# Performance work log

Hardware: AMD Instinct MI355X
Metric: run time of the kernel (lower is better)

Reference implementation:

```python
import jax, jax.numpy as jnp
import numpy as np
from jax.experimental.ode import odeint

B, N, D, META, H, OUT = 512, 64, 4, 4, 512, 1
RTOL, ATOL = 1e-3, 1e-5


def setup_inputs() -> dict:
    key = jax.random.key(0)
    ks = jax.random.split(key, 20)
    # x channel 0 = strictly increasing event times per sample (TIME), rest randn
    dt = jax.random.uniform(ks[0], (B, N), dtype=jnp.float32) * 0.1 + 0.01
    times = jnp.cumsum(dt, axis=1)
    feats = jax.random.normal(ks[1], (B, N, D - 1), dtype=jnp.float32)
    x = jnp.concatenate([times[..., None], feats], axis=-1)
    meta = jax.random.normal(ks[2], (B, META), dtype=jnp.float32)
    eps = jax.random.normal(ks[3], (B, H), dtype=jnp.float32)

    DIN = D + META
    s_in = 1.0 / np.sqrt(DIN)
    s_h = 1.0 / np.sqrt(H)
    p = {
        # GRU (torch layout: gates [r, z, n] stacked)
        'gru_Wih': jax.random.normal(ks[4], (3 * H, DIN), jnp.float32) * s_in,
        'gru_Whh': jax.random.normal(ks[5], (3 * H, H), jnp.float32) * s_h,
        'gru_bih': jax.random.normal(ks[6], (3 * H,), jnp.float32) * s_h,
        'gru_bhh': jax.random.normal(ks[7], (3 * H,), jnp.float32) * s_h,
        # encoder head: Linear(H,H) -> ReLU -> Linear(H,2H)
        'enc_W1': jax.random.normal(ks[8], (H, H), jnp.float32) * s_h,
        'enc_b1': jax.random.normal(ks[9], (H,), jnp.float32) * s_h,
        'enc_W2': jax.random.normal(ks[10], (2 * H, H), jnp.float32) * s_h,
        'enc_b2': jax.random.normal(ks[11], (2 * H,), jnp.float32) * s_h,
        # ODE drift net: Linear(H,H) -> SELU -> Linear(H,H); scaled mild for stable dynamics
        'ode_W1': jax.random.normal(ks[12], (H, H), jnp.float32) * (0.5 * s_h),
        'ode_b1': jax.random.normal(ks[13], (H,), jnp.float32) * 0.05,
        'ode_W2': jax.random.normal(ks[14], (H, H), jnp.float32) * (0.5 * s_h),
        'ode_b2': jax.random.normal(ks[15], (H,), jnp.float32) * 0.05,
        # output head: Linear(H+META, OUT)
        'fc_W': jax.random.normal(ks[16], (OUT, H + META), jnp.float32) / np.sqrt(H + META),
        'fc_b': jax.random.normal(ks[17], (OUT,), jnp.float32) / np.sqrt(H + META),
    }
    return {'x': x, 'meta': meta, 'eps': eps, **p}


def _gru_last(xm, Wih, Whh, bih, bhh):
    # xm: (B, N, DIN) -> final hidden state (B, H), torch nn.GRU equations
    def step(h, x_t):
        gi = x_t @ Wih.T + bih            # (B, 3H)
        gh = h @ Whh.T + bhh              # (B, 3H)
        i_r, i_z, i_n = jnp.split(gi, 3, axis=-1)
        h_r, h_z, h_n = jnp.split(gh, 3, axis=-1)
        r = jax.nn.sigmoid(i_r + h_r)
        z = jax.nn.sigmoid(i_z + h_z)
        n = jnp.tanh(i_n + r * h_n)
        return (1.0 - z) * n + z * h, None
    h0 = jnp.zeros((xm.shape[0], Whh.shape[1]), xm.dtype)
    h, _ = jax.lax.scan(step, h0, jnp.swapaxes(xm, 0, 1))
    return h


def reference(x, meta, eps, gru_Wih, gru_Whh, gru_bih, gru_bhh,
              enc_W1, enc_b1, enc_W2, enc_b2,
              ode_W1, ode_b1, ode_W2, ode_b2, fc_W, fc_b):
    times = x[:, :, 0]                                        # (B, N)
    metat = jnp.broadcast_to(meta[:, None, :], (x.shape[0], x.shape[1], meta.shape[1]))
    xm = jnp.concatenate([x, metat], axis=-1)                 # (B, N, D+META)
    h = _gru_last(xm, gru_Wih, gru_Whh, gru_bih, gru_bhh)     # (B, H)
    out = jax.nn.relu(h @ enc_W1.T + enc_b1) @ enc_W2.T + enc_b2
    mean, std = out[:, :H], out[:, H:]
    z0 = eps * std + mean                                     # reparameterized sample

    def drift(z, t, W1, b1, W2, b2):
        return jax.nn.selu(z @ W1.T + b1) @ W2.T + b2

    def solve_one(z0_b, t_b):
        return odeint(drift, z0_b, t_b, ode_W1, ode_b1, ode_W2, ode_b2,
                      rtol=RTOL, atol=ATOL)                   # (N, H)

    solves = jax.vmap(solve_one)(z0, times)                   # (B, N, H)
    latent = jnp.concatenate([solves[:, -1, :], meta], axis=-1)
    return latent @ fc_W.T + fc_b                             # (B, OUT)
```

## Files before the change

kernel.cpp:

```cpp
#include <hip/hip_runtime.h>
#include <math.h>

constexpr int Bsz  = 512;
constexpr int Nseq = 64;
constexpr int DX   = 4;
constexpr int MET  = 4;
constexpr int Hd   = 512;
constexpr int H3d  = 1536;

constexpr int PJ = 520;
constexpr int CK = 8;

constexpr float RTOL_C = 1e-3f;
constexpr float ATOL_C = 1e-5f;

constexpr float SB10 = (float)(1.0/5.0);
constexpr float SB20 = (float)(3.0/40.0),  SB21 = (float)(9.0/40.0);
constexpr float SB30 = (float)(44.0/45.0), SB31 = (float)(-56.0/15.0), SB32 = (float)(32.0/9.0);
constexpr float SB40 = (float)(19372.0/6561.0), SB41 = (float)(-25360.0/2187.0),
                SB42 = (float)(64448.0/6561.0), SB43 = (float)(-212.0/729.0);
constexpr float SB50 = (float)(9017.0/3168.0),  SB51 = (float)(-355.0/33.0),
                SB52 = (float)(46732.0/5247.0), SB53 = (float)(49.0/176.0),
                SB54 = (float)(-5103.0/18656.0);
constexpr float CS0 = (float)(35.0/384.0), CS2 = (float)(500.0/1113.0),
                CS3 = (float)(125.0/192.0), CS4 = (float)(-2187.0/6784.0),
                CS5 = (float)(11.0/84.0);
constexpr float CE0 = (float)(35.0/384.0 - 1951.0/21600.0);
constexpr float CE2 = (float)(500.0/1113.0 - 22642.0/50085.0);
constexpr float CE3 = (float)(125.0/192.0 - 451.0/720.0);
constexpr float CE4 = (float)(-2187.0/6784.0 + 12231.0/42400.0);
constexpr float CE5 = (float)(11.0/84.0 - 649.0/6300.0);
constexpr float CE6 = (float)(-1.0/60.0);
constexpr float CM0 = (float)(6025192743.0/30085553152.0/2.0);
constexpr float CM2 = (float)(51252292925.0/65400821598.0/2.0);
constexpr float CM3 = (float)(-2691868925.0/45128329728.0/2.0);
constexpr float CM4 = (float)(187940372067.0/1594534317056.0/2.0);
constexpr float CM5 = (float)(-1776094331.0/19743644256.0/2.0);
constexpr float CM6 = (float)(11237099.0/235043384.0/2.0);

__device__ __forceinline__ float selu_f(float v) {
  const float scl = 1.0507009873554805f;
  const float alp = 1.6732632423543772f;
  float e = v > 0.f ? v : alp * expm1f(v);
  return scl * e;
}
__device__ __forceinline__ float sigmoid_f(float v) {
  return 1.f / (1.f + expf(-v));
}

__global__ __launch_bounds__(256) void pack_all_kernel(
    const float* __restrict__ gWhh, const float* __restrict__ gWih,
    const float* __restrict__ eW1,  const float* __restrict__ eW2,
    const float* __restrict__ oW1,  const float* __restrict__ oW2,
    float* __restrict__ WhhP, float* __restrict__ WihT,
    float* __restrict__ eW1P, float* __restrict__ eW2P,
    float* __restrict__ oW1P, float* __restrict__ oW2P)
{
  int i = blockIdx.x * 256 + threadIdx.x;
  if (i < 786432) {
    const int r = i >> 9, k = i & 511;
    const int gate = r >> 9, jr = r & 511;
    WhhP[(((k >> 2) * 3 + gate) * PJ + jr) * 4 + (k & 3)] = gWhh[i];
  } else if (i < 798720) {
    const int ii = i - 786432;
    const int r = ii >> 3, c = ii & 7;
    WihT[c * H3d + r] = gWih[ii];
  } else if (i < 1060864) {
    const int ii = i - 798720;
    const int r = ii >> 9, k = ii & 511;
    eW1P[(k >> 2) * (Hd * 4) + r * 4 + (k & 3)] = eW1[ii];
  } else if (i < 1585152) {
    const int ii = i - 1060864;
    const int r = ii >> 9, k = ii & 511;
    eW2P[(k >> 2) * (1024 * 4) + r * 4 + (k & 3)] = eW2[ii];
  } else if (i < 1847296) {
    const int ii = i - 1585152;
    const int r = ii >> 9, k = ii & 511;
    oW1P[((k >> 2) * PJ + r) * 4 + (k & 3)] = oW1[ii];
  } else if (i < 2109440) {
    const int ii = i - 1847296;
    const int r = ii >> 9, k = ii & 511;
    oW2P[((k >> 2) * PJ + r) * 4 + (k & 3)] = oW2[ii];
  }
}

__global__ __launch_bounds__(512) void gru_step_kernel(
    const float* __restrict__ x, const float* __restrict__ meta,
    const float* __restrict__ WihT, const float* __restrict__ WhhP,
    const float* __restrict__ bih, const float* __restrict__ bhh,
    const float* __restrict__ h_in, float* __restrict__ h_out, int t)
{
  __shared__ __align__(16) float hs[16 * Hd];
  __shared__ __align__(16) float4 wlds[2][CK * 2 * 64];
  const int tid = threadIdx.x;
  const int jl  = tid & 63;
  const int rg  = tid >> 6;
  const int j0  = blockIdx.y * 64;
  const int j   = j0 + jl;
  const int b0  = blockIdx.x * 16;

  const float4* __restrict__ W4 = (const float4*)WhhP;

  for (int i = tid; i < 16 * Hd / 4; i += 512)
    *(float4*)&hs[i * 4] = *(const float4*)&h_in[b0 * Hd + i * 4];

  auto stage = [&](int c, int buf) {
    for (int i = tid; i < CK * 2 * 64; i += 512) {
      const int kk   = i >> 7;
      const int rem  = i & 127;
      const int gate = rem >> 6;
      const int col  = rem & 63;
      wlds[buf][i] = W4[((c * CK + kk) * 3 + gate) * PJ + j0 + col];
    }
  };
  stage(0, 0);
  __syncthreads();

  float ar0 = 0.f, az0 = 0.f, an0 = 0.f;
  float ar1 = 0.f, az1 = 0.f, an1 = 0.f;
  constexpr int NCHUNK = (Hd / 4) / CK;
  for (int c = 0; c < NCHUNK; ++c) {
    const int buf = c & 1;
    if (c + 1 < NCHUNK) stage(c + 1, buf ^ 1);
    const float4* __restrict__ wl = &wlds[buf][0];
#pragma unroll
    for (int kk = 0; kk < CK; ++kk) {
      const int k4 = c * CK + kk;
      const float4 wr = wl[(kk * 2 + 0) * 64 + jl];
      const float4 wz = wl[(kk * 2 + 1) * 64 + jl];
      const float4 wn = W4[(k4 * 3 + 2) * PJ + j];
      const float4 h0 = *(const float4*)&hs[(rg * 2 + 0) * Hd + k4 * 4];
      const float4 h1 = *(const float4*)&hs[(rg * 2 + 1) * Hd + k4 * 4];
      ar0 += wr.x * h0.x + wr.y * h0.y + wr.z * h0.z + wr.w * h0.w;
      az0 += wz.x * h0.x + wz.y * h0.y + wz.z * h0.z + wz.w * h0.w;
      an0 += wn.x * h0.x + wn.y * h0.y + wn.z * h0.z + wn.w * h0.w;
      ar1 += wr.x * h1.x + wr.y * h1.y + wr.z * h1.z + wr.w * h1.w;
      az1 += wz.x * h1.x + wz.y * h1.y + wz.z * h1.z + wz.w * h1.w;
      an1 += wn.x * h1.x + wn.y * h1.y + wn.z * h1.z + wn.w * h1.w;
    }
    __syncthreads();
  }

  const float bihr = bih[j], bihz = bih[512 + j], bihn = bih[1024 + j];
  const float bhhr = bhh[j], bhhz = bhh[512 + j], bhhn = bhh[1024 + j];
  float wir[8], wiz[8], win[8];
#pragma unroll
  for (int kk = 0; kk < 8; ++kk) {
    wir[kk] = WihT[kk * H3d + j];
    wiz[kk] = WihT[kk * H3d + 512 + j];
    win[kk] = WihT[kk * H3d + 1024 + j];
  }

#pragma unroll
  for (int m = 0; m < 2; ++m) {
    const int bl = rg * 2 + m;
    const int b  = b0 + bl;
    const float4 xv = *(const float4*)&x[(b * Nseq + t) * DX];
    const float4 mv = *(const float4*)&meta[b * MET];
    float xm[8] = { xv.x, xv.y, xv.z, xv.w, mv.x, mv.y, mv.z, mv.w };
    float gr = bihr, gz = bihz, gn = bihn;
#pragma unroll
    for (int kk = 0; kk < 8; ++kk) {
      gr += xm[kk] * wir[kk];
      gz += xm[kk] * wiz[kk];
      gn += xm[kk] * win[kk];
    }
    const float ghr = (m ? ar1 : ar0) + bhhr;
    const float ghz = (m ? az1 : az0) + bhhz;
    const float ghn = (m ? an1 : an0) + bhhn;
    const float r = sigmoid_f(gr + ghr);
    const float z = sigmoid_f(gz + ghz);
    const float n = tanhf(gn + r * ghn);
    const float hold = hs[bl * Hd + j];
    h_out[b * Hd + j] = (1.f - z) * n + z * hold;
  }
}

__global__ __launch_bounds__(256) void gemm_relu_kernel(
    const float* __restrict__ A, const float* __restrict__ WP,
    const float* __restrict__ bias, float* __restrict__ Cout)
{
  __shared__ __align__(16) float as[16 * Hd];
  const int tid  = threadIdx.x;
  const int jl   = tid & 63;
  const int bsub = tid >> 6;
  const int j    = blockIdx.y * 64 + jl;
  const int b0   = blockIdx.x * 16;

  for (int i = tid; i < 16 * Hd; i += 256) as[i] = A[b0 * Hd + i];
  __syncthreads();

  float acc[4] = {0.f, 0.f, 0.f, 0.f};
#pragma unroll 2
  for (int k4 = 0; k4 < Hd / 4; ++k4) {
    const float4 w = *(const float4*)&WP[(k4 * Hd + j) * 4];
#pragma unroll
    for (int m = 0; m < 4; ++m) {
      const float4 av = *(const float4*)&as[(bsub * 4 + m) * Hd + k4 * 4];
      acc[m] += w.x * av.x + w.y * av.y + w.z * av.z + w.w * av.w;
    }
  }
  const float bj = bias[j];
#pragma unroll
  for (int m = 0; m < 4; ++m) {
    const int b = b0 + bsub * 4 + m;
    float v = acc[m] + bj;
    Cout[b * Hd + j] = v > 0.f ? v : 0.f;
  }
}

__global__ __launch_bounds__(256) void enc2_z0_kernel(
    const float* __restrict__ O1, const float* __restrict__ W2P,
    const float* __restrict__ b2, const float* __restrict__ eps,
    float* __restrict__ z0)
{
  __shared__ __align__(16) float as[16 * Hd];
  const int tid  = threadIdx.x;
  const int jl   = tid & 63;
  const int bsub = tid >> 6;
  const int j    = blockIdx.y * 64 + jl;
  const int b0   = blockIdx.x * 16;

  for (int i = tid; i < 16 * Hd; i += 256) as[i] = O1[b0 * Hd + i];
  __syncthreads();

  float am[4] = {0.f, 0.f, 0.f, 0.f};
  float asd[4] = {0.f, 0.f, 0.f, 0.f};
#pragma unroll 2
  for (int k4 = 0; k4 < Hd / 4; ++k4) {
    const float4 wm = *(const float4*)&W2P[(k4 * 1024 + j) * 4];
    const float4 ws = *(const float4*)&W2P[(k4 * 1024 + 512 + j) * 4];
#pragma unroll
    for (int m = 0; m < 4; ++m) {
      const float4 av = *(const float4*)&as[(bsub * 4 + m) * Hd + k4 * 4];
      am[m]  += wm.x * av.x + wm.y * av.y + wm.z * av.z + wm.w * av.w;
      asd[m] += ws.x * av.x + ws.y * av.y + ws.z * av.z + ws.w * av.w;
    }
  }
  const float bm = b2[j], bs = b2[512 + j];
#pragma unroll
  for (int m = 0; m < 4; ++m) {
    const int b = b0 + bsub * 4 + m;
    const float mean = am[m] + bm;
    const float sd   = asd[m] + bs;
    z0[b * Hd + j] = eps[b * Hd + j] * sd + mean;
  }
}

__global__ __launch_bounds__(512) void ode_fc_kernel(
    const float* __restrict__ x, const float* __restrict__ meta,
    const float* __restrict__ z0in,
    const float* __restrict__ W1P, const float* __restrict__ b1v,
    const float* __restrict__ W2P, const float* __restrict__ b2v,
    const float* __restrict__ fcW, const float* __restrict__ fcb,
    float* __restrict__ outp)
{
  constexpr int GE = 2;
  __shared__ __align__(16) float zsh[GE][Hd];
  __shared__ float red[8 * GE];
  const int tid = threadIdx.x;
  const int j   = tid;
  const int bg0 = blockIdx.x * GE;

  const float b1r = b1v[j];
  const float b2r = b2v[j];

  auto drift = [&](const float (&in)[2], float (&out)[2]) {
    __syncthreads();
    zsh[0][j] = in[0];
    zsh[1][j] = in[1];
    __syncthreads();
    float u0 = b1r, u1 = b1r;
#pragma unroll 4
    for (int k4 = 0; k4 < Hd / 4; ++k4) {
      const float4 w  = *(const float4*)&W1P[(k4 * PJ + j) * 4];
      const float4 z0 = *(const float4*)&zsh[0][k4 * 4];
      const float4 z1 = *(const float4*)&zsh[1][k4 * 4];
      u0 += w.x * z0.x + w.y * z0.y + w.z * z0.z + w.w * z0.w;
      u1 += w.x * z1.x + w.y * z1.y + w.z * z1.z + w.w * z1.w;
    }
    u0 = selu_f(u0); u1 = selu_f(u1);
    __syncthreads();
    zsh[0][j] = u0;
    zsh[1][j] = u1;
    __syncthreads();
    float v0 = b2r, v1 = b2r;
#pragma unroll 4
    for (int k4 = 0; k4 < Hd / 4; ++k4) {
      const float4 w  = *(const float4*)&W2P[(k4 * PJ + j) * 4];
      const float4 z0 = *(const float4*)&zsh[0][k4 * 4];
      const float4 z1 = *(const float4*)&zsh[1][k4 * 4];
      v0 += w.x * z0.x + w.y * z0.y + w.z * z0.z + w.w * z0.w;
      v1 += w.x * z1.x + w.y * z1.y + w.z * z1.z + w.w * z1.w;
    }
    out[0] = v0; out[1] = v1;
  };

  auto blocksum = [&](float (&v)[GE], float (&s)[GE]) {
#pragma unroll
    for (int off = 32; off > 0; off >>= 1) {
#pragma unroll
      for (int g = 0; g < GE; ++g) v[g] += __shfl_down(v[g], off);
    }
    __syncthreads();
    if ((tid & 63) == 0) {
      const int w = tid >> 6;
#pragma unroll
      for (int g = 0; g < GE; ++g) red[w * GE + g] = v[g];
    }
    __syncthreads();
#pragma unroll
    for (int g = 0; g < GE; ++g) {
      float t = 0.f;
#pragma unroll
      for (int w = 0; w < 8; ++w) t += red[w * GE + g];
      s[g] = t;
    }
  };

  float y[2], f[2], py[2], pf[2], ym[2];
  float tcur[GE], dtv[GE], tfin[GE], ptv[GE], pdt[GE];
  bool act[GE];

#pragma unroll
  for (int g = 0; g < GE; ++g) {
    y[g]    = z0in[(bg0 + g) * Hd + j];
    tcur[g] = x[((bg0 + g) * Nseq + 0) * DX];
    tfin[g] = x[((bg0 + g) * Nseq + (Nseq - 1)) * DX];
  }

  drift(y, f);

  float sc[2], q0[GE], q1[GE];
#pragma unroll
  for (int l = 0; l < 2; ++l) {
    sc[l] = ATOL_C + RTOL_C * fabsf(y[l]);
    const float a = y[l] / sc[l], b = f[l] / sc[l];
    q0[l] = a * a;
    q1[l] = b * b;
  }
  float d0s[GE], d1s[GE];
  blocksum(q0, d0s);
  blocksum(q1, d1s);
  float h0[GE];
#pragma unroll
  for (int g = 0; g < GE; ++g) {
    const float d0 = sqrtf(d0s[g]), d1 = sqrtf(d1s[g]);
    h0[g] = (d0 < 1e-5f || d1 < 1e-5f) ? 1e-6f : 0.01f * d0 / d1;
  }
  float yin[2], f1h[2];
#pragma unroll
  for (int l = 0; l < 2; ++l) yin[l] = y[l] + h0[l] * f[l];
  drift(yin, f1h);
  float q2[GE];
#pragma unroll
  for (int l = 0; l < 2; ++l) {
    const float dd = (f1h[l] - f[l]) / sc[l];
    q2[l] = dd * dd;
  }
  float d2s[GE];
  blocksum(q2, d2s);
#pragma unroll
  for (int g = 0; g < GE; ++g) {
    const float d1 = sqrtf(d1s[g]);
    const float d2 = sqrtf(d2s[g]) / h0[g];
    const float h1 = (d1 <= 1e-15f && d2 <= 1e-15f)
                 ? fmaxf(1e-6f, h0[g] * 1e-3f)
                 : powf(0.01f / (d1 + d2), 0.2f);
    dtv[g] = fminf(100.f * h0[g], h1);
    ptv[g] = tcur[g]; pdt[g] = dtv[g];
    act[g] = (tcur[g] < tfin[g]) && (dtv[g] > 0.f);
  }
#pragma unroll
  for (int l = 0; l < 2; ++l) { py[l] = y[l]; pf[l] = f[l]; ym[l] = y[l]; }

  float k2[2], k3[2], k4v[2], k5[2], k6[2], k7[2], y1v[2];
  for (int iter = 0; iter < 4000; ++iter) {
    if (!(act[0] || act[1])) break;

#pragma unroll
    for (int l = 0; l < 2; ++l) yin[l] = y[l] + dtv[l] * (SB10 * f[l]);
    drift(yin, k2);

#pragma unroll
    for (int l = 0; l < 2; ++l)
      yin[l] = y[l] + dtv[l] * (SB20 * f[l] + SB21 * k2[l]);
    drift(yin, k3);

#pragma unroll
    for (int l = 0; l < 2; ++l)
      yin[l] = y[l] + dtv[l] * (SB30 * f[l] + SB31 * k2[l] + SB32 * k3[l]);
    drift(yin, k4v);

#pragma unroll
    for (int l = 0; l < 2; ++l)
      yin[l] = y[l] + dtv[l] * (SB40 * f[l] + SB41 * k2[l] + SB42 * k3[l] + SB43 * k4v[l]);
    drift(yin, k5);

#pragma unroll
    for (int l = 0; l < 2; ++l)
      yin[l] = y[l] + dtv[l] * (SB50 * f[l] + SB51 * k2[l] + SB52 * k3[l] + SB53 * k4v[l] + SB54 * k5[l]);
    drift(yin, k6);

#pragma unroll
    for (int l = 0; l < 2; ++l)
      y1v[l] = y[l] + dtv[l] * (CS0 * f[l] + CS2 * k3[l] + CS3 * k4v[l] + CS4 * k5[l] + CS5 * k6[l]);
    drift(y1v, k7);

    float rs[GE];
#pragma unroll
    for (int l = 0; l < 2; ++l) {
      const float yerr = dtv[l] * (CE0 * f[l] + CE2 * k3[l] + CE3 * k4v[l] + CE4 * k5[l] + CE5 * k6[l] + CE6 * k7[l]);
      const float tol = ATOL_C + RTOL_C * fmaxf(fabsf(y[l]), fabsf(y1v[l]));
      const float r = yerr / tol;
      rs[l] = r * r;
    }
    float rsum[GE];
    blocksum(rs, rsum);

    bool acc[GE];
#pragma unroll
    for (int g = 0; g < GE; ++g)
      acc[g] = act[g] && (sqrtf(rsum[g] * (1.0f / Hd)) <= 1.0f);

#pragma unroll
    for (int l = 0; l < 2; ++l) {
      if (acc[l]) {
        ym[l] = y[l] + dtv[l] * (CM0 * f[l] + CM2 * k3[l] + CM3 * k4v[l] + CM4 * k5[l] + CM5 * k6[l] + CM6 * k7[l]);
        py[l] = y[l]; pf[l] = f[l];
        y[l] = y1v[l]; f[l] = k7[l];
      }
    }
#pragma unroll
    for (int g = 0; g < GE; ++g) {
      if (!act[g]) continue;
      const float er = sqrtf(rsum[g] * (1.0f / Hd));
      if (acc[g]) {
        ptv[g] = tcur[g]; pdt[g] = dtv[g];
        tcur[g] = tcur[g] + dtv[g];
      }
      float dtn;
      if (er == 0.0f) {
        dtn = dtv[g] * 10.0f;
      } else {
        const float dfac = (er < 1.0f) ? 1.0f : 0.2f;
        const float fac = fminf(10.0f, fmaxf(0.9f * powf(er, -0.2f), dfac));
        dtn = dtv[g] * fac;
      }
      dtv[g] = fmaxf(dtn, 0.0f);
      act[g] = (tcur[g] < tfin[g]) && (dtv[g] > 0.0f);
    }
  }

  const float fcw = fcW[j];
  float s[GE];
#pragma unroll
  for (int l = 0; l < 2; ++l) {
    const float denom = tcur[l] - ptv[l];
    const float xr = (tfin[l] - ptv[l]) / denom;
    const float dy0 = pdt[l] * pf[l];
    const float dy1 = pdt[l] * f[l];
    const float aa = -2.f * dy0 + 2.f * dy1 - 8.f * py[l] - 8.f * y[l] + 16.f * ym[l];
    const float bb =  5.f * dy0 - 3.f * dy1 + 18.f * py[l] + 14.f * y[l] - 32.f * ym[l];
    const float cc = -4.f * dy0 + 1.f * dy1 - 11.f * py[l] - 5.f * y[l] + 16.f * ym[l];
    const float dd = dy0;
    const float ee = py[l];
    const float yf = (((aa * xr + bb) * xr + cc) * xr + dd) * xr + ee;
    s[l] = yf * fcw;
  }
  float ssum[GE];
  blocksum(s, ssum);
  if (tid == 0) {
#pragma unroll
    for (int g = 0; g < GE; ++g) {
      float o = ssum[g] + fcb[0];
#pragma unroll
      for (int m = 0; m < MET; ++m) o += meta[(bg0 + g) * MET + m] * fcW[Hd + m];
      outp[bg0 + g] = o;
    }
  }
}

extern "C" void kernel_launch(void* const* d_in, const int* in_sizes, int n_in,
                              void* d_out, int out_size, void* d_ws, size_t ws_size,
                              hipStream_t stream)
{
  (void)in_sizes; (void)n_in; (void)out_size; (void)ws_size;

  const float* x    = (const float*)d_in[0];
  const float* meta = (const float*)d_in[1];
  const float* eps  = (const float*)d_in[2];
  const float* gWih = (const float*)d_in[3];
  const float* gWhh = (const float*)d_in[4];
  const float* gbih = (const float*)d_in[5];
  const float* gbhh = (const float*)d_in[6];
  const float* eW1  = (const float*)d_in[7];
  const float* eb1  = (const float*)d_in[8];
  const float* eW2  = (const float*)d_in[9];
  const float* eb2  = (const float*)d_in[10];
  const float* oW1  = (const float*)d_in[11];
  const float* ob1  = (const float*)d_in[12];
  const float* oW2  = (const float*)d_in[13];
  const float* ob2  = (const float*)d_in[14];
  const float* fcW  = (const float*)d_in[15];
  const float* fcb  = (const float*)d_in[16];
  float* out = (float*)d_out;
  float* ws  = (float*)d_ws;

  float* WhhP = ws + 0;
  float* WihT = ws + 798720;
  float* eW1P = ws + 811008;
  float* eW2P = ws + 1073152;
  float* oW1P = ws + 1597440;
  float* oW2P = ws + 1863680;
  float* hA   = ws + 2129920;
  float* hB   = ws + 2392064;

  pack_all_kernel<<<(2109440 + 255) / 256, 256, 0, stream>>>(
      gWhh, gWih, eW1, eW2, oW1, oW2, WhhP, WihT, eW1P, eW2P, oW1P, oW2P);
  hipMemsetAsync(hA, 0, (size_t)Bsz * Hd * sizeof(float), stream);

  dim3 ggrid(32, 8);
  for (int t = 0; t < Nseq; ++t) {
    const float* hin = (t & 1) ? hB : hA;
    float* hout      = (t & 1) ? hA : hB;
    gru_step_kernel<<<ggrid, 512, 0, stream>>>(x, meta, WihT, WhhP, gbih, gbhh, hin, hout, t);
  }
  dim3 egrid(32, 8);
  gemm_relu_kernel<<<egrid, 256, 0, stream>>>(hA, eW1P, eb1, hB);
  enc2_z0_kernel<<<egrid, 256, 0, stream>>>(hB, eW2P, eb2, eps, hA);
  ode_fc_kernel<<<Bsz / 2, 512, 0, stream>>>(x, meta, hA, oW1P, ob1, oW2P, ob2, fcW, fcb, out);
}
```

Before: 2.752 ms.

## Repack GRU recurrent weights per column tile and drop LDS staging

The GRU hidden weights are repacked into a layout that is contiguous per 64-column tile, with k4, gate and column as the inner dimensions. The step kernel then reads all three gate weights straight from global memory instead of double-buffering the r and z gates through LDS. This removes the LDS staging copies and the barrier after every chunk. The cost is that the eight row-groups in a block now each read the same weights from global memory, relying on cache to absorb the duplicate traffic.

```diff
diff --git a/kernel.cpp b/kernel.cpp
--- a/kernel.cpp
+++ b/kernel.cpp
@@ -9,7 +9,6 @@
 constexpr int H3d  = 1536;
 
 constexpr int PJ = 520;
-constexpr int CK = 8;
 
 constexpr float RTOL_C = 1e-3f;
 constexpr float ATOL_C = 1e-5f;
@@ -52,7 +51,7 @@
     const float* __restrict__ gWhh, const float* __restrict__ gWih,
     const float* __restrict__ eW1,  const float* __restrict__ eW2,
     const float* __restrict__ oW1,  const float* __restrict__ oW2,
-    float* __restrict__ WhhP, float* __restrict__ WihT,
+    float* __restrict__ WhhB, float* __restrict__ WihT,
     float* __restrict__ eW1P, float* __restrict__ eW2P,
     float* __restrict__ oW1P, float* __restrict__ oW2P)
 {
@@ -60,7 +59,9 @@
   if (i < 786432) {
     const int r = i >> 9, k = i & 511;
     const int gate = r >> 9, jr = r & 511;
-    WhhP[(((k >> 2) * 3 + gate) * PJ + jr) * 4 + (k & 3)] = gWhh[i];
+    const int jt = jr >> 6, jl = jr & 63;
+    const int k4 = k >> 2, kk = k & 3;
+    WhhB[((((jt * 128 + k4) * 3 + gate) * 64) + jl) * 4 + kk] = gWhh[i];
   } else if (i < 798720) {
     const int ii = i - 786432;
     const int r = ii >> 3, c = ii & 7;
@@ -86,59 +87,39 @@
 
 __global__ __launch_bounds__(512) void gru_step_kernel(
     const float* __restrict__ x, const float* __restrict__ meta,
-    const float* __restrict__ WihT, const float* __restrict__ WhhP,
+    const float* __restrict__ WihT, const float* __restrict__ WhhB,
     const float* __restrict__ bih, const float* __restrict__ bhh,
     const float* __restrict__ h_in, float* __restrict__ h_out, int t)
 {
   __shared__ __align__(16) float hs[16 * Hd];
-  __shared__ __align__(16) float4 wlds[2][CK * 2 * 64];
   const int tid = threadIdx.x;
   const int jl  = tid & 63;
   const int rg  = tid >> 6;
-  const int j0  = blockIdx.y * 64;
-  const int j   = j0 + jl;
+  const int jt  = blockIdx.y;
+  const int j   = jt * 64 + jl;
   const int b0  = blockIdx.x * 16;
 
-  const float4* __restrict__ W4 = (const float4*)WhhP;
+  const float4* __restrict__ W4 = (const float4*)WhhB + (size_t)jt * 128 * 3 * 64;
 
   for (int i = tid; i < 16 * Hd / 4; i += 512)
     *(float4*)&hs[i * 4] = *(const float4*)&h_in[b0 * Hd + i * 4];
-
-  auto stage = [&](int c, int buf) {
-    for (int i = tid; i < CK * 2 * 64; i += 512) {
-      const int kk   = i >> 7;
-      const int rem  = i & 127;
-      const int gate = rem >> 6;
-      const int col  = rem & 63;
-      wlds[buf][i] = W4[((c * CK + kk) * 3 + gate) * PJ + j0 + col];
-    }
-  };
-  stage(0, 0);
   __syncthreads();
 
   float ar0 = 0.f, az0 = 0.f, an0 = 0.f;
   float ar1 = 0.f, az1 = 0.f, an1 = 0.f;
-  constexpr int NCHUNK = (Hd / 4) / CK;
-  for (int c = 0; c < NCHUNK; ++c) {
-    const int buf = c & 1;
-    if (c + 1 < NCHUNK) stage(c + 1, buf ^ 1);
-    const float4* __restrict__ wl = &wlds[buf][0];
-#pragma unroll
-    for (int kk = 0; kk < CK; ++kk) {
-      const int k4 = c * CK + kk;
-      const float4 wr = wl[(kk * 2 + 0) * 64 + jl];
-      const float4 wz = wl[(kk * 2 + 1) * 64 + jl];
-      const float4 wn = W4[(k4 * 3 + 2) * PJ + j];
-      const float4 h0 = *(const float4*)&hs[(rg * 2 + 0) * Hd + k4 * 4];
-      const float4 h1 = *(const float4*)&hs[(rg * 2 + 1) * Hd + k4 * 4];
-      ar0 += wr.x * h0.x + wr.y * h0.y + wr.z * h0.z + wr.w * h0.w;
-      az0 += wz.x * h0.x + wz.y * h0.y + wz.z * h0.z + wz.w * h0.w;
-      an0 += wn.x * h0.x + wn.y * h0.y + wn.z * h0.z + wn.w * h0.w;
-      ar1 += wr.x * h1.x + wr.y * h1.y + wr.z * h1.z + wr.w * h1.w;
-      az1 += wz.x * h1.x + wz.y * h1.y + wz.z * h1.z + wz.w * h1.w;
-      an1 += wn.x * h1.x + wn.y * h1.y + wn.z * h1.z + wn.w * h1.w;
-    }
-    __syncthreads();
+#pragma unroll 4
+  for (int k4 = 0; k4 < Hd / 4; ++k4) {
+    const float4 wr = W4[(k4 * 3 + 0) * 64 + jl];
+    const float4 wz = W4[(k4 * 3 + 1) * 64 + jl];
+    const float4 wn = W4[(k4 * 3 + 2) * 64 + jl];
+    const float4 h0 = *(const float4*)&hs[(rg * 2 + 0) * Hd + k4 * 4];
+    const float4 h1 = *(const float4*)&hs[(rg * 2 + 1) * Hd + k4 * 4];
+    ar0 += wr.x * h0.x + wr.y * h0.y + wr.z * h0.z + wr.w * h0.w;
+    az0 += wz.x * h0.x + wz.y * h0.y + wz.z * h0.z + wz.w * h0.w;
+    an0 += wn.x * h0.x + wn.y * h0.y + wn.z * h0.z + wn.w * h0.w;
+    ar1 += wr.x * h1.x + wr.y * h1.y + wr.z * h1.z + wr.w * h1.w;
+    az1 += wz.x * h1.x + wz.y * h1.y + wz.z * h1.z + wz.w * h1.w;
+    an1 += wn.x * h1.x + wn.y * h1.y + wn.z * h1.z + wn.w * h1.w;
   }
 
   const float bihr = bih[j], bihz = bih[512 + j], bihn = bih[1024 + j];
@@ -507,24 +488,24 @@
   float* out = (float*)d_out;
   float* ws  = (float*)d_ws;
 
-  float* WhhP = ws + 0;
-  float* WihT = ws + 798720;
-  float* eW1P = ws + 811008;
-  float* eW2P = ws + 1073152;
-  float* oW1P = ws + 1597440;
-  float* oW2P = ws + 1863680;
-  float* hA   = ws + 2129920;
-  float* hB   = ws + 2392064;
+  float* WhhB = ws + 0;
+  float* WihT = ws + 786432;
+  float* eW1P = ws + 798720;
+  float* eW2P = ws + 1060864;
+  float* oW1P = ws + 1585152;
+  float* oW2P = ws + 1851392;
+  float* hA   = ws + 2117632;
+  float* hB   = ws + 2379776;
 
   pack_all_kernel<<<(2109440 + 255) / 256, 256, 0, stream>>>(
-      gWhh, gWih, eW1, eW2, oW1, oW2, WhhP, WihT, eW1P, eW2P, oW1P, oW2P);
+      gWhh, gWih, eW1, eW2, oW1, oW2, WhhB, WihT, eW1P, eW2P, oW1P, oW2P);
   hipMemsetAsync(hA, 0, (size_t)Bsz * Hd * sizeof(float), stream);
 
   dim3 ggrid(32, 8);
   for (int t = 0; t < Nseq; ++t) {
     const float* hin = (t & 1) ? hB : hA;
     float* hout      = (t & 1) ? hA : hB;
-    gru_step_kernel<<<ggrid, 512, 0, stream>>>(x, meta, WihT, WhhP, gbih, gbhh, hin, hout, t);
+    gru_step_kernel<<<ggrid, 512, 0, stream>>>(x, meta, WihT, WhhB, gbih, gbhh, hin, hout, t);
   }
   dim3 egrid(32, 8);
   gemm_relu_kernel<<<egrid, 256, 0, stream>>>(hA, eW1P, eb1, hB);
```

Result: faster. 2.369 ms (-13.9%).
